# Optimization experiments

Hardware: AMD Instinct MI355X
Metric: run time of the kernel (lower is better)

## Reference

```python
import jax, jax.numpy as jnp
import numpy as np

N, IN, C, H, NC, E, G = 4096, 16, 128, 2, 4, 131072, 64
EPS = 1e-5


def setup_inputs() -> dict:
    key = jax.random.key(0)
    ks = jax.random.split(key, 12)
    def rn(k, shape, scale=0.05):
        return jax.random.normal(k, shape, dtype=jnp.float32) * scale
    return dict(
        x=rn(ks[0], (N, IN), 1.0),
        edge_index=jax.random.randint(ks[1], (2, E), 0, N, dtype=jnp.int32),
        batch=jnp.sort(jax.random.randint(ks[2], (N,), 0, G, dtype=jnp.int32)),
        proj_W=rn(ks[3], (IN, C)), proj_b=jnp.zeros((C,), jnp.float32),
        gcn_W=rn(ks[4], (2, C, C)), gcn_b=jnp.zeros((2, C), jnp.float32),
        attn_qkv_w=rn(ks[5], (2, 3 * C, C)), attn_qkv_b=jnp.zeros((2, 3 * C), jnp.float32),
        attn_out_w=rn(ks[6], (2, C, C)), attn_out_b=jnp.zeros((2, C), jnp.float32),
        bn_gamma=jnp.ones((2, 3, C), jnp.float32), bn_beta=jnp.zeros((2, 3, C), jnp.float32),
        mlp_W1=rn(ks[7], (2, C, 2 * C)), mlp_b1=jnp.zeros((2, 2 * C), jnp.float32),
        mlp_W2=rn(ks[8], (2, 2 * C, C)), mlp_b2=jnp.zeros((2, C), jnp.float32),
        lin_W=rn(ks[9], (C, NC)), lin_b=jnp.zeros((NC,), jnp.float32),
    )


def _bn(h, g, b):
    # PyG BatchNorm (training-mode stats over the node dim, biased var)
    mu = jnp.mean(h, axis=0)
    var = jnp.mean((h - mu) ** 2, axis=0)
    return (h - mu) * jax.lax.rsqrt(var + EPS) * g + b


def _gcn(h_in, W, b, src, dst):
    # GCNConv: x' = D^-1/2 (A+I) D^-1/2 (x W) + b
    h = h_in @ W
    deg = jnp.zeros((N,), h.dtype).at[dst].add(1.0) + 1.0  # +1 self loop
    dinv = jax.lax.rsqrt(deg)
    coef = dinv[src] * dinv[dst]                           # [E]
    out = jax.ops.segment_sum(h[src] * coef[:, None], dst, num_segments=N)
    out = out + h * (dinv * dinv)[:, None]                 # self-loop term
    return out + b


def _mha(x, wqkv, bqkv, wout, bout):
    # batch=None in the source => attention over all N nodes as one sequence
    qkv = x @ wqkv.T + bqkv                                # [N,3C]
    q, k, v = jnp.split(qkv, 3, axis=-1)
    dh = C // H
    q = q.reshape(N, H, dh) * (dh ** -0.5)
    k = k.reshape(N, H, dh)
    v = v.reshape(N, H, dh)
    a = jax.nn.softmax(jnp.einsum('nhd,mhd->hnm', q, k), axis=-1)  # [H,N,N]
    o = jnp.einsum('hnm,mhd->nhd', a, v).reshape(N, C)
    return o @ wout.T + bout


def _forward(x, proj_W, proj_b, gcn_W, gcn_b, attn_qkv_w, attn_qkv_b,
             attn_out_w, attn_out_b, bn_gamma, bn_beta, mlp_W1, mlp_b1,
             mlp_W2, mlp_b2, lin_W, lin_b, edge_index, batch):
    src, dst = edge_index[0], edge_index[1]
    h = x @ proj_W + proj_b
    for l in range(2):  # two structurally-distinct GPS layers
        hl = _bn(_gcn(h, gcn_W[l], gcn_b[l], src, dst) + h, bn_gamma[l, 0], bn_beta[l, 0])
        ha = _bn(_mha(h, attn_qkv_w[l], attn_qkv_b[l], attn_out_w[l], attn_out_b[l]) + h,
                 bn_gamma[l, 1], bn_beta[l, 1])
        o = hl + ha
        m = jax.nn.relu(o @ mlp_W1[l] + mlp_b1[l]) @ mlp_W2[l] + mlp_b2[l]
        h = _bn(o + m, bn_gamma[l, 2], bn_beta[l, 2])
        if l == 0:
            h = jax.nn.relu(h)
    ssum = jax.ops.segment_sum(h, batch, num_segments=G)
    cnt = jax.ops.segment_sum(jnp.ones((N,), h.dtype), batch, num_segments=G)
    pooled = ssum / jnp.maximum(cnt, 1.0)[:, None]
    return pooled @ lin_W + lin_b


def reference(x, edge_index, batch, proj_W, proj_b, gcn_W, gcn_b,
              attn_qkv_w, attn_qkv_b, attn_out_w, attn_out_b,
              bn_gamma, bn_beta, mlp_W1, mlp_b1, mlp_W2, mlp_b2,
              lin_W, lin_b):
    return _forward(x, proj_W, proj_b, gcn_W, gcn_b, attn_qkv_w, attn_qkv_b,
                    attn_out_w, attn_out_b, bn_gamma, bn_beta, mlp_W1, mlp_b1,
                    mlp_W2, mlp_b2, lin_W, lin_b, edge_index, batch)
```

## Files before the change

### kernel.cpp

```cpp
#include <hip/hip_runtime.h>
#include <hip/hip_bf16.h>


constexpr int N_  = 4096;
constexpr int IN_ = 16;
constexpr int C_  = 128;
constexpr int E_  = 131072;
constexpr int G_  = 64;
constexpr float EPSV = 1e-5f;
constexpr int SP_ = 8;

typedef unsigned short u16;
typedef __attribute__((ext_vector_type(8))) short bf16x8;
typedef __attribute__((ext_vector_type(8))) unsigned short u16x8;
typedef __attribute__((ext_vector_type(4))) float f32x4;

__device__ inline u16 f2bf(float f) {
  union { __hip_bfloat16 b; u16 u; } v;
  v.b = __float2bfloat16(f);
  return v.u;
}
__device__ inline float bf2f(u16 s) {
  union { unsigned u; float f; } v; v.u = ((unsigned)s) << 16;
  return v.f;
}

__global__ __launch_bounds__(256) void prol_k(const float* __restrict__ x,
                                              const float* __restrict__ projW,
                                              const float* __restrict__ projB,
                                              float* __restrict__ h,
                                              const float* __restrict__ gcnW,
                                              const float* __restrict__ qkvW,
                                              const float* __restrict__ outW,
                                              const float* __restrict__ w1,
                                              const float* __restrict__ w2,
                                              u16* __restrict__ Wh,
                                              u16* __restrict__ Wl,
                                              const int* __restrict__ ei,
                                              int* __restrict__ cnt) {
  const int bx = blockIdx.x;
  const int tid = threadIdx.x;
  if (bx < 2048) {
    int idx = bx * 256 + tid;
    int n = idx >> 7, c = idx & 127;
    float acc = projB[c];
#pragma unroll
    for (int k = 0; k < IN_; ++k) acc = fmaf(x[n * IN_ + k], projW[k * C_ + c], acc);
    h[idx] = acc;
    return;
  }
  if (bx >= 2336) {
    int e = (bx - 2336) * 256 + tid;
    atomicAdd(&cnt[ei[E_ + e]], 1);
    return;
  }
  int wb = bx - 2048;
  int l = wb / 144, b = wb % 144;
  const float* src; int dstOff, K, M, trans;
  if (b < 16)       { src = gcnW + l * 16384; dstOff = 0;      K = 128; M = 128; trans = 0; }
  else if (b < 64)  { src = qkvW + l * 49152; dstOff = 16384;  K = 128; M = 0;   trans = 1; b -= 16; }
  else if (b < 80)  { src = outW + l * 16384; dstOff = 65536;  K = 128; M = 0;   trans = 1; b -= 64; }
  else if (b < 112) { src = w1 + l * 32768;   dstOff = 81920;  K = 128; M = 256; trans = 0; b -= 80; }
  else              { src = w2 + l * 32768;   dstOff = 114688; K = 256; M = 128; trans = 0; b -= 112; }
  dstOff += l * 147456;
  int d = b * 1024 + tid * 4;
  float v[4];
  if (trans) {
    const float4 f = *(const float4*)&src[d];
    v[0] = f.x; v[1] = f.y; v[2] = f.z; v[3] = f.w;
  } else {
    int ks = (K == 256) ? 8 : 7;
    int n = d >> ks, k = d & (K - 1);
#pragma unroll
    for (int j = 0; j < 4; ++j) v[j] = src[(size_t)(k + j) * M + n];
  }
  ushort4 hv, lv;
  u16* hp = (u16*)&hv; u16* lp = (u16*)&lv;
#pragma unroll
  for (int j = 0; j < 4; ++j) {
    u16 hh = f2bf(v[j]); hp[j] = hh; lp[j] = f2bf(v[j] - bf2f(hh));
  }
  *(ushort4*)&Wh[dstOff + d] = hv;
  *(ushort4*)&Wl[dstOff + d] = lv;
}

__global__ __launch_bounds__(256) void scan_k(const int* __restrict__ cnt,
                                              int* __restrict__ rowptr,
                                              int* __restrict__ cursor,
                                              float* __restrict__ dinv) {
  __shared__ int part[256];
  const int t = threadIdx.x;
  int v[16], s = 0;
#pragma unroll
  for (int i = 0; i < 16; ++i) { v[i] = cnt[t * 16 + i]; s += v[i]; }
  part[t] = s;
  __syncthreads();
  if (t == 0) {
    int run = 0;
    for (int i = 0; i < 256; ++i) { int x = part[i]; part[i] = run; run += x; }
  }
  __syncthreads();
  int off = part[t];
#pragma unroll
  for (int i = 0; i < 16; ++i) {
    int n = t * 16 + i;
    rowptr[n] = off; cursor[n] = off;
    dinv[n] = rsqrtf((float)v[i] + 1.0f);
    off += v[i];
  }
  if (t == 0) rowptr[N_] = E_;
}

__global__ __launch_bounds__(256) void mgemm_dual_k(const float* __restrict__ A,
                                                    const u16* __restrict__ Bh,
                                                    const u16* __restrict__ Bl,
                                                    const float* __restrict__ qkvB,
                                                    float* __restrict__ t0,
                                                    u16* __restrict__ Qg,
                                                    u16* __restrict__ Kg,
                                                    u16* __restrict__ Vtg,
                                                    const int* __restrict__ ei,
                                                    int* __restrict__ cursor,
                                                    int* __restrict__ csr) {
  constexpr int LD = 72, K = 128;
  __shared__ u16 Ah[64 * LD], Al[64 * LD], Bsh[64 * LD], Bsl[64 * LD];
  const int bx = blockIdx.x;
  const int tid = threadIdx.x;
  if (bx >= 512) {
    int e = (bx - 512) * 256 + tid;
    int d = ei[E_ + e];
    int slot = atomicAdd(&cursor[d], 1);
    csr[slot] = ei[e];
    return;
  }
  const int row0 = (bx >> 3) * 64, col0 = (bx & 7) * 64;
  const int wv = tid >> 6, ln = tid & 63, quad = ln >> 4, c = ln & 15;
  f32x4 acc[4];
#pragma unroll
  for (int i = 0; i < 4; ++i) acc[i] = (f32x4){0.f, 0.f, 0.f, 0.f};

  for (int kt = 0; kt < K; kt += 64) {
    __syncthreads();
#pragma unroll
    for (int i = 0; i < 2; ++i) {
      int ch = tid + i * 256, r = ch >> 3, part = ch & 7;
      const float4 f0 = *(const float4*)&A[(size_t)(row0 + r) * K + kt + part * 8];
      const float4 f1 = *(const float4*)&A[(size_t)(row0 + r) * K + kt + part * 8 + 4];
      float fv[8] = {f0.x, f0.y, f0.z, f0.w, f1.x, f1.y, f1.z, f1.w};
      __attribute__((aligned(16))) u16 hb[8], lb[8];
#pragma unroll
      for (int j = 0; j < 8; ++j) {
        u16 hh = f2bf(fv[j]); hb[j] = hh; lb[j] = f2bf(fv[j] - bf2f(hh));
      }
      *(u16x8*)&Ah[r * LD + part * 8] = *(u16x8*)hb;
      *(u16x8*)&Al[r * LD + part * 8] = *(u16x8*)lb;
      size_t bo = (size_t)(col0 + r) * K + kt + part * 8;
      *(u16x8*)&Bsh[r * LD + part * 8] = *(const u16x8*)&Bh[bo];
      *(u16x8*)&Bsl[r * LD + part * 8] = *(const u16x8*)&Bl[bo];
    }
    __syncthreads();
#pragma unroll
    for (int kq = 0; kq < 2; ++kq) {
      bf16x8 ah = *(const bf16x8*)&Ah[(wv * 16 + c) * LD + kq * 32 + quad * 8];
      bf16x8 al = *(const bf16x8*)&Al[(wv * 16 + c) * LD + kq * 32 + quad * 8];
#pragma unroll
      for (int cb = 0; cb < 4; ++cb) {
        bf16x8 bh = *(const bf16x8*)&Bsh[(cb * 16 + c) * LD + kq * 32 + quad * 8];
        bf16x8 bl = *(const bf16x8*)&Bsl[(cb * 16 + c) * LD + kq * 32 + quad * 8];
        acc[cb] = __builtin_amdgcn_mfma_f32_16x16x32_bf16(al, bh, acc[cb], 0, 0, 0);
        acc[cb] = __builtin_amdgcn_mfma_f32_16x16x32_bf16(ah, bl, acc[cb], 0, 0, 0);
        acc[cb] = __builtin_amdgcn_mfma_f32_16x16x32_bf16(ah, bh, acc[cb], 0, 0, 0);
      }
    }
  }

  const int cls = bx & 7;
  if (cls < 2) {
#pragma unroll
    for (int cb = 0; cb < 4; ++cb)
#pragma unroll
      for (int r = 0; r < 4; ++r) {
        int rr = row0 + wv * 16 + quad * 4 + r;
        t0[(size_t)rr * 128 + col0 + cb * 16 + c] = acc[cb][r];
      }
  } else if (cls < 6) {
    const int isQ = cls < 4, hd = cls & 1;
    const float sc = isQ ? 0.125f : 1.0f;
    u16* dst = isQ ? Qg : Kg;
#pragma unroll
    for (int cb = 0; cb < 4; ++cb) {
      int d = cb * 16 + c;
      float qb = qkvB[col0 - 128 + d];
#pragma unroll
      for (int r = 0; r < 4; ++r) {
        int rr = row0 + wv * 16 + quad * 4 + r;
        dst[((size_t)(hd * N_ + rr)) * 64 + d] = f2bf((acc[cb][r] + qb) * sc);
      }
    }
  } else {
    const int hd = cls & 1;
    u16* vtile = Ah;
    __syncthreads();
#pragma unroll
    for (int cb = 0; cb < 4; ++cb) {
      int d = cb * 16 + c;
      float vb = qkvB[col0 - 128 + d];
#pragma unroll
      for (int r = 0; r < 4; ++r)
        vtile[(wv * 16 + quad * 4 + r) * LD + d] = f2bf(acc[cb][r] + vb);
    }
    __syncthreads();
    int d = tid >> 2, j = tid & 3;
    __attribute__((aligned(16))) u16 buf[16];
#pragma unroll
    for (int m = 0; m < 16; ++m) buf[m] = vtile[(j * 16 + m) * LD + d];
    size_t o = ((size_t)(hd * 64 + d)) * N_ + row0 + j * 16;
    *(u16x8*)&Vtg[o]     = *(u16x8*)&buf[0];
    *(u16x8*)&Vtg[o + 8] = *(u16x8*)&buf[8];
  }
}

__global__ __launch_bounds__(256) void mgemm_k(const float* __restrict__ A,
                                               const u16* __restrict__ Bh,
                                               const u16* __restrict__ Bl,
                                               const float* __restrict__ bias,
                                               float* __restrict__ Cout,
                                               int K, int Ncols, int relu,
                                               const float* __restrict__ resid,
                                               float* __restrict__ sums) {
  constexpr int LD = 72;
  __shared__ u16 Ah[64 * LD], Al[64 * LD], Bsh[64 * LD], Bsl[64 * LD];
  const int tid = threadIdx.x;
  const int row0 = blockIdx.y * 64, col0 = blockIdx.x * 64;
  const int wv = tid >> 6, ln = tid & 63, quad = ln >> 4, c = ln & 15;
  f32x4 acc[4];
#pragma unroll
  for (int i = 0; i < 4; ++i) acc[i] = (f32x4){0.f, 0.f, 0.f, 0.f};

  for (int kt = 0; kt < K; kt += 64) {
    __syncthreads();
#pragma unroll
    for (int i = 0; i < 2; ++i) {
      int ch = tid + i * 256, r = ch >> 3, part = ch & 7;
      const float4 f0 = *(const float4*)&A[(size_t)(row0 + r) * K + kt + part * 8];
      const float4 f1 = *(const float4*)&A[(size_t)(row0 + r) * K + kt + part * 8 + 4];
      float fv[8] = {f0.x, f0.y, f0.z, f0.w, f1.x, f1.y, f1.z, f1.w};
      __attribute__((aligned(16))) u16 hb[8], lb[8];
#pragma unroll
      for (int j = 0; j < 8; ++j) {
        u16 hh = f2bf(fv[j]); hb[j] = hh; lb[j] = f2bf(fv[j] - bf2f(hh));
      }
      *(u16x8*)&Ah[r * LD + part * 8] = *(u16x8*)hb;
      *(u16x8*)&Al[r * LD + part * 8] = *(u16x8*)lb;
      size_t bo = (size_t)(col0 + r) * K + kt + part * 8;
      *(u16x8*)&Bsh[r * LD + part * 8] = *(const u16x8*)&Bh[bo];
      *(u16x8*)&Bsl[r * LD + part * 8] = *(const u16x8*)&Bl[bo];
    }
    __syncthreads();
#pragma unroll
    for (int kq = 0; kq < 2; ++kq) {
      bf16x8 ah = *(const bf16x8*)&Ah[(wv * 16 + c) * LD + kq * 32 + quad * 8];
      bf16x8 al = *(const bf16x8*)&Al[(wv * 16 + c) * LD + kq * 32 + quad * 8];
#pragma unroll
      for (int cb = 0; cb < 4; ++cb) {
        bf16x8 bh = *(const bf16x8*)&Bsh[(cb * 16 + c) * LD + kq * 32 + quad * 8];
        bf16x8 bl = *(const bf16x8*)&Bsl[(cb * 16 + c) * LD + kq * 32 + quad * 8];
        acc[cb] = __builtin_amdgcn_mfma_f32_16x16x32_bf16(al, bh, acc[cb], 0, 0, 0);
        acc[cb] = __builtin_amdgcn_mfma_f32_16x16x32_bf16(ah, bl, acc[cb], 0, 0, 0);
        acc[cb] = __builtin_amdgcn_mfma_f32_16x16x32_bf16(ah, bh, acc[cb], 0, 0, 0);
      }
    }
  }
#pragma unroll
  for (int cb = 0; cb < 4; ++cb) {
    float s = 0.0f, s2 = 0.0f;
#pragma unroll
    for (int r = 0; r < 4; ++r) {
      int rr = row0 + wv * 16 + quad * 4 + r;
      int cc = col0 + cb * 16 + c;
      float o = acc[cb][r] + (bias ? bias[cc] : 0.0f);
      if (resid) o += resid[(size_t)rr * Ncols + cc];
      if (relu) o = fmaxf(o, 0.0f);
      Cout[(size_t)rr * Ncols + cc] = o;
      s += o; s2 = fmaf(o, o, s2);
    }
    if (sums) {
      s  += __shfl_xor(s, 16);  s  += __shfl_xor(s, 32);
      s2 += __shfl_xor(s2, 16); s2 += __shfl_xor(s2, 32);
      if (quad == 0) {
        int cc = col0 + cb * 16 + c;
        atomicAdd(&sums[cc], s);
        atomicAdd(&sums[C_ + cc], s2);
      }
    }
  }
}

__global__ __launch_bounds__(256) void mgemm_attn_k(const float* __restrict__ attnP,
                                                    const float* __restrict__ accLp,
                                                    const u16* __restrict__ Bh,
                                                    const u16* __restrict__ Bl,
                                                    const float* __restrict__ bias,
                                                    float* __restrict__ Cout,
                                                    const float* __restrict__ resid,
                                                    float* __restrict__ sums) {
  constexpr int LD = 72, K = 128;
  __shared__ u16 Ah[64 * LD], Al[64 * LD], Bsh[64 * LD], Bsl[64 * LD];
  const int tid = threadIdx.x;
  const int row0 = blockIdx.y * 64, col0 = blockIdx.x * 64;
  const int wv = tid >> 6, ln = tid & 63, quad = ln >> 4, c = ln & 15;
  f32x4 acc[4];
#pragma unroll
  for (int i = 0; i < 4; ++i) acc[i] = (f32x4){0.f, 0.f, 0.f, 0.f};

  for (int kt = 0; kt < K; kt += 64) {
    const int head = kt >> 6;
    __syncthreads();
#pragma unroll
    for (int i = 0; i < 2; ++i) {
      int ch = tid + i * 256, r = ch >> 3, part = ch & 7;
      float lsum = 0.0f;
#pragma unroll
      for (int sp = 0; sp < SP_; ++sp) lsum += accLp[(sp * 2 + head) * N_ + row0 + r];
      float invl = 1.0f / lsum;
      float fv[8] = {0.f, 0.f, 0.f, 0.f, 0.f, 0.f, 0.f, 0.f};
#pragma unroll
      for (int sp = 0; sp < SP_; ++sp) {
        const float* p = &attnP[((size_t)sp * N_ + row0 + r) * C_ + kt + part * 8];
        const float4 f0 = *(const float4*)p;
        const float4 f1 = *(const float4*)(p + 4);
        fv[0] += f0.x; fv[1] += f0.y; fv[2] += f0.z; fv[3] += f0.w;
        fv[4] += f1.x; fv[5] += f1.y; fv[6] += f1.z; fv[7] += f1.w;
      }
      __attribute__((aligned(16))) u16 hb[8], lb[8];
#pragma unroll
      for (int j = 0; j < 8; ++j) {
        float f = fv[j] * invl;
        u16 hh = f2bf(f); hb[j] = hh; lb[j] = f2bf(f - bf2f(hh));
      }
      *(u16x8*)&Ah[r * LD + part * 8] = *(u16x8*)hb;
      *(u16x8*)&Al[r * LD + part * 8] = *(u16x8*)lb;
      size_t bo = (size_t)(col0 + r) * K + kt + part * 8;
      *(u16x8*)&Bsh[r * LD + part * 8] = *(const u16x8*)&Bh[bo];
      *(u16x8*)&Bsl[r * LD + part * 8] = *(const u16x8*)&Bl[bo];
    }
    __syncthreads();
#pragma unroll
    for (int kq = 0; kq < 2; ++kq) {
      bf16x8 ah = *(const bf16x8*)&Ah[(wv * 16 + c) * LD + kq * 32 + quad * 8];
      bf16x8 al = *(const bf16x8*)&Al[(wv * 16 + c) * LD + kq * 32 + quad * 8];
#pragma unroll
      for (int cb = 0; cb < 4; ++cb) {
        bf16x8 bh = *(const bf16x8*)&Bsh[(cb * 16 + c) * LD + kq * 32 + quad * 8];
        bf16x8 bl = *(const bf16x8*)&Bsl[(cb * 16 + c) * LD + kq * 32 + quad * 8];
        acc[cb] = __builtin_amdgcn_mfma_f32_16x16x32_bf16(al, bh, acc[cb], 0, 0, 0);
        acc[cb] = __builtin_amdgcn_mfma_f32_16x16x32_bf16(ah, bl, acc[cb], 0, 0, 0);
        acc[cb] = __builtin_amdgcn_mfma_f32_16x16x32_bf16(ah, bh, acc[cb], 0, 0, 0);
      }
    }
  }
#pragma unroll
  for (int cb = 0; cb < 4; ++cb) {
    float s = 0.0f, s2 = 0.0f;
#pragma unroll
    for (int r = 0; r < 4; ++r) {
      int rr = row0 + wv * 16 + quad * 4 + r;
      int cc = col0 + cb * 16 + c;
      float o = acc[cb][r] + bias[cc] + resid[(size_t)rr * 128 + cc];
      Cout[(size_t)rr * 128 + cc] = o;
      s += o; s2 = fmaf(o, o, s2);
    }
    s  += __shfl_xor(s, 16);  s  += __shfl_xor(s, 32);
    s2 += __shfl_xor(s2, 16); s2 += __shfl_xor(s2, 32);
    if (quad == 0) {
      int cc = col0 + cb * 16 + c;
      atomicAdd(&sums[cc], s);
      atomicAdd(&sums[C_ + cc], s2);
    }
  }
}

__global__ __launch_bounds__(256) void branch_k(const u16* __restrict__ Qg,
                                                const u16* __restrict__ Kg,
                                                const u16* __restrict__ Vtg,
                                                float* __restrict__ attnP,
                                                float* __restrict__ accLp,
                                                const int* __restrict__ rowptr,
                                                const int* __restrict__ csr,
                                                const float* __restrict__ hw,
                                                const float* __restrict__ dinv,
                                                const float* __restrict__ gbias,
                                                const float* __restrict__ hres,
                                                float* __restrict__ t1,
                                                float* __restrict__ sums0) {
  constexpr int LD = 72;
  __shared__ __attribute__((aligned(16))) u16 smem[3 * 64 * LD];
  const int tid = threadIdx.x;
  const int bx = blockIdx.x;

  if (bx & 1) {
    const int b = bx >> 1;
    const int wq = tid >> 6, lane = tid & 63;
    const int n = b * 4 + wq;
    float* ls  = (float*)smem;
    float* ls2 = ls + 512;
    const float din = dinv[n];
    float a0 = fmaf(hw[(size_t)n * C_ + lane], din * din,
                    gbias[lane] + hres[(size_t)n * C_ + lane]);
    float a1 = fmaf(hw[(size_t)n * C_ + lane + 64], din * din,
                    gbias[lane + 64] + hres[(size_t)n * C_ + lane + 64]);
    const int e1 = rowptr[n + 1];
    for (int e = rowptr[n]; e < e1; ++e) {
      int si = csr[e];
      float w = dinv[si] * din;
      a0 = fmaf(hw[(size_t)si * C_ + lane], w, a0);
      a1 = fmaf(hw[(size_t)si * C_ + lane + 64], w, a1);
    }
    t1[(size_t)n * C_ + lane]      = a0;
    t1[(size_t)n * C_ + lane + 64] = a1;
    ls[wq * 128 + lane]       = a0;  ls[wq * 128 + lane + 64]  = a1;
    ls2[wq * 128 + lane]      = a0 * a0;
    ls2[wq * 128 + lane + 64] = a1 * a1;
    __syncthreads();
    if (tid < 128) {
      float s  = ls[tid]  + ls[tid + 128]  + ls[tid + 256]  + ls[tid + 384];
      float s2 = ls2[tid] + ls2[tid + 128] + ls2[tid + 256] + ls2[tid + 384];
      atomicAdd(&sums0[tid], s);
      atomicAdd(&sums0[C_ + tid], s2);
    }
    return;
  }

  u16* Ks  = smem;
  u16* Vts = smem + 64 * LD;
  u16* Ps  = smem + 2 * 64 * LD;
  const int fb = bx >> 1;
  const int head = fb >> 9, sp = (fb >> 6) & 7, q0 = (fb & 63) * 64;
  const int wv = tid >> 6, ln = tid & 63, quad = ln >> 4, c = ln & 15;
  const int KPS = N_ / SP_;

  bf16x8 qf[2];
#pragma unroll
  for (int kq = 0; kq < 2; ++kq)
    qf[kq] = *(const bf16x8*)&Qg[((size_t)(head * N_ + q0 + wv * 16 + c)) * 64 + kq * 32 + quad * 8];

  f32x4 O[4];
#pragma unroll
  for (int i = 0; i < 4; ++i) O[i] = (f32x4){0.f, 0.f, 0.f, 0.f};
  float l4[4] = {0.f, 0.f, 0.f, 0.f};
  u16* Pw = &Ps[wv * 16 * LD];

  for (int it = 0; it < KPS / 64; ++it) {
    const int k0 = sp * KPS + it * 64;
    __syncthreads();
#pragma unroll
    for (int i = 0; i < 2; ++i) {
      int ch = tid + i * 256, row = ch >> 3, part = ch & 7;
      *(u16x8*)&Ks[row * LD + part * 8] =
          *(const u16x8*)&Kg[((size_t)(head * N_ + k0 + row)) * 64 + part * 8];
      *(u16x8*)&Vts[row * LD + part * 8] =
          *(const u16x8*)&Vtg[((size_t)(head * 64 + row)) * N_ + k0 + part * 8];
    }
    __syncthreads();

#pragma unroll
    for (int kb = 0; kb < 4; ++kb) {
      f32x4 s = (f32x4){0.f, 0.f, 0.f, 0.f};
#pragma unroll
      for (int kq = 0; kq < 2; ++kq) {
        bf16x8 b = *(const bf16x8*)&Ks[(kb * 16 + c) * LD + kq * 32 + quad * 8];
        s = __builtin_amdgcn_mfma_f32_16x16x32_bf16(qf[kq], b, s, 0, 0, 0);
      }
#pragma unroll
      for (int r = 0; r < 4; ++r) {
        u16 ph = f2bf(__expf(s[r] - 8.0f));
        l4[r] += bf2f(ph);
        Pw[(quad * 4 + r) * LD + kb * 16 + c] = ph;
      }
    }
#pragma unroll
    for (int db = 0; db < 4; ++db) {
#pragma unroll
      for (int kq = 0; kq < 2; ++kq) {
        bf16x8 a = *(const bf16x8*)&Pw[c * LD + kq * 32 + quad * 8];
        bf16x8 b = *(const bf16x8*)&Vts[(db * 16 + c) * LD + kq * 32 + quad * 8];
        O[db] = __builtin_amdgcn_mfma_f32_16x16x32_bf16(a, b, O[db], 0, 0, 0);
      }
    }
  }

#pragma unroll
  for (int r = 0; r < 4; ++r) {
#pragma unroll
    for (int off = 1; off < 16; off <<= 1) l4[r] += __shfl_xor(l4[r], off);
  }

#pragma unroll
  for (int db = 0; db < 4; ++db)
#pragma unroll
    for (int r = 0; r < 4; ++r) {
      int q = q0 + wv * 16 + quad * 4 + r;
      attnP[((size_t)sp * N_ + q) * C_ + head * 64 + db * 16 + c] = O[db][r];
    }
  if (c == 0) {
#pragma unroll
    for (int r = 0; r < 4; ++r)
      accLp[(sp * 2 + head) * N_ + q0 + wv * 16 + quad * 4 + r] = l4[r];
  }
}

__global__ __launch_bounds__(256) void bn_finapply2_k(const float* __restrict__ t0,
                                                      const float* __restrict__ t1,
                                                      const float* __restrict__ sums1,
                                                      const float* __restrict__ sums0,
                                                      const float* __restrict__ g1,
                                                      const float* __restrict__ b1v,
                                                      const float* __restrict__ g0,
                                                      const float* __restrict__ b0v,
                                                      float* __restrict__ ob) {
  __shared__ float scl1[128], shf1[128], scl0[128], shf0[128];
  const int t = threadIdx.x;
  if (t < 128) {
    float mu = sums1[t] * (1.0f / N_);
    float var = sums1[C_ + t] * (1.0f / N_) - mu * mu;
    float sc = rsqrtf(var + EPSV) * g1[t];
    scl1[t] = sc; shf1[t] = fmaf(-mu, sc, b1v[t]);
    mu = sums0[t] * (1.0f / N_);
    var = sums0[C_ + t] * (1.0f / N_) - mu * mu;
    sc = rsqrtf(var + EPSV) * g0[t];
    scl0[t] = sc; shf0[t] = fmaf(-mu, sc, b0v[t]);
  }
  __syncthreads();
  int idx = blockIdx.x * 256 + t;
  int c = idx & 127;
  ob[idx] = fmaf(t0[idx], scl1[c], shf1[c]) + fmaf(t1[idx], scl0[c], shf0[c]);
}

__global__ __launch_bounds__(256) void bn_finapply_k(const float* __restrict__ A,
                                                     const float* __restrict__ sums,
                                                     const float* __restrict__ g,
                                                     const float* __restrict__ b,
                                                     float* __restrict__ outp, int relu,
                                                     const int* __restrict__ batch,
                                                     float* __restrict__ pooled) {
  __shared__ float s_scl[128], s_shf[128];
  const int t = threadIdx.x;
  if (t < 128) {
    float mu = sums[t] * (1.0f / N_);
    float var = sums[C_ + t] * (1.0f / N_) - mu * mu;
    float sc = rsqrtf(var + EPSV) * g[t];
    s_scl[t] = sc;
    s_shf[t] = fmaf(-mu, sc, b[t]);
  }
  __syncthreads();
  int idx = blockIdx.x * 256 + t;
  int c = idx & 127;
  float v = fmaf(A[idx], s_scl[c], s_shf[c]);
  if (relu) v = fmaxf(v, 0.0f);
  outp[idx] = v;
  if (pooled) {
    int n = idx >> 7;
    atomicAdd(&pooled[(size_t)batch[n] * C_ + c], v);
  }
}

__global__ __launch_bounds__(256) void final_k(const float* __restrict__ pooled,
                                               const int* __restrict__ batch,
                                               const float* __restrict__ W,
                                               const float* __restrict__ b,
                                               float* __restrict__ out) {
  int t = threadIdx.x;
  int g = t >> 2, j = t & 3;
  int lo = 0, hi = N_;
  while (lo < hi) { int m = (lo + hi) >> 1; if (batch[m] < g) lo = m + 1; else hi = m; }
  int st = lo; lo = 0; hi = N_;
  while (lo < hi) { int m = (lo + hi) >> 1; if (batch[m] < g + 1) lo = m + 1; else hi = m; }
  float inv = 1.0f / fmaxf((float)(lo - st), 1.0f);
  float acc = b[j];
  for (int c = 0; c < C_; ++c) acc = fmaf(pooled[(size_t)g * C_ + c] * inv, W[c * 4 + j], acc);
  out[t] = acc;
}

extern "C" void kernel_launch(void* const* d_in, const int* in_sizes, int n_in,
                              void* d_out, int out_size, void* d_ws, size_t ws_size,
                              hipStream_t stream) {
  const float* x     = (const float*)d_in[0];
  const int*   ei    = (const int*)d_in[1];
  const int*   batch = (const int*)d_in[2];
  const float* projW = (const float*)d_in[3];
  const float* projB = (const float*)d_in[4];
  const float* gcnW  = (const float*)d_in[5];
  const float* gcnB  = (const float*)d_in[6];
  const float* qkvW  = (const float*)d_in[7];
  const float* qkvB  = (const float*)d_in[8];
  const float* outW  = (const float*)d_in[9];
  const float* outB  = (const float*)d_in[10];
  const float* bnG   = (const float*)d_in[11];
  const float* bnB   = (const float*)d_in[12];
  const float* w1    = (const float*)d_in[13];
  const float* b1    = (const float*)d_in[14];
  const float* w2    = (const float*)d_in[15];
  const float* b2    = (const float*)d_in[16];
  const float* linW  = (const float*)d_in[17];
  const float* linB  = (const float*)d_in[18];
  float* out = (float*)d_out;

  const size_t NC = (size_t)N_ * C_;
  const size_t HB = (size_t)2 * N_ * 64;
  float* ws   = (float*)d_ws;
  float* h    = ws;
  float* t0   = ws + 1 * NC;
  float* t1   = ws + 2 * NC;
  float* ob   = ws + 3 * NC;
  u16* Qg  = (u16*)(ws + 4 * NC);
  u16* Kg  = Qg + HB;
  u16* Vtg = Kg + HB;
  float* attnP = ws + 6 * NC;
  float* m1b   = attnP;
  float* accLp = ws + (6 + SP_) * NC;
  float* sums  = accLp + 2 * SP_ * N_;
  float* pooled = sums + 6 * 256;
  int*   icnt = (int*)(pooled + (size_t)G_ * C_);
  float* dinv = (float*)(icnt + N_);
  int*   rowptr = (int*)(dinv + N_);
  int*   cursor = rowptr + N_ + 1;
  int*   csr    = cursor + N_;
  u16*   Wh = (u16*)(csr + E_);
  u16*   Wl = Wh + 2 * 147456;

  const dim3 b256(256);

  hipMemsetAsync(sums, 0, (6 * 256 + (size_t)G_ * C_ + N_) * sizeof(float), stream);

  prol_k<<<2848, b256, 0, stream>>>(x, projW, projB, h, gcnW, qkvW, outW,
                                    w1, w2, Wh, Wl, ei, icnt);
  scan_k<<<1, b256, 0, stream>>>(icnt, rowptr, cursor, dinv);

  for (int l = 0; l < 2; ++l) {
    const size_t WL = (size_t)l * 147456;
    float* sums0 = sums + (l * 3 + 0) * 256;
    float* sums1 = sums + (l * 3 + 1) * 256;
    float* sums2 = sums + (l * 3 + 2) * 256;

    mgemm_dual_k<<<(l == 0) ? 1024 : 512, b256, 0, stream>>>(
        h, Wh + WL, Wl + WL, qkvB + l * 384, t0, Qg, Kg, Vtg, ei, cursor, csr);
    branch_k<<<2048, b256, 0, stream>>>(Qg, Kg, Vtg, attnP, accLp,
                                        rowptr, csr, t0, dinv, gcnB + l * C_,
                                        h, t1, sums0);
    mgemm_attn_k<<<dim3(2, 64), b256, 0, stream>>>(attnP, accLp,
                                                   Wh + WL + 65536, Wl + WL + 65536,
                                                   outB + l * C_, t0, h, sums1);
    bn_finapply2_k<<<(int)(NC / 256), b256, 0, stream>>>(
        t0, t1, sums1, sums0,
        bnG + (l * 3 + 1) * C_, bnB + (l * 3 + 1) * C_,
        bnG + (l * 3 + 0) * C_, bnB + (l * 3 + 0) * C_, ob);
    mgemm_k<<<dim3(4, 64), b256, 0, stream>>>(ob, Wh + WL + 81920, Wl + WL + 81920,
                                              b1 + l * 256, m1b, 128, 256, 1,
                                              nullptr, nullptr);
    mgemm_k<<<dim3(2, 64), b256, 0, stream>>>(m1b, Wh + WL + 114688, Wl + WL + 114688,
                                              b2 + l * C_, t0, 256, 128, 0,
                                              ob, sums2);
    bn_finapply_k<<<(int)(NC / 256), b256, 0, stream>>>(
        t0, sums2, bnG + (l * 3 + 2) * C_, bnB + (l * 3 + 2) * C_, h,
        (l == 0) ? 1 : 0, batch, (l == 1) ? pooled : nullptr);
  }

  final_k<<<1, 256, 0, stream>>>(pooled, batch, linW, linB, out);
}
```

Baseline: 318.4 us.

## Keep attention P in registers via transposed MFMA and bpermute, vectorize output stores

The attention path computes S^T by swapping the MFMA operands, so each lane holds probabilities for a single query. These are packed as bf16 pairs and redistributed with ds_bpermute to form the B operand of the PV MFMA, replacing the LDS round trip for P and shrinking shared memory. The per-row exp sum becomes one scalar per lane reduced with two shuffles. Output tiles are transposed through LDS so attnP is written with float4 stores. The GCN gather loop is also unrolled by four to get more loads in flight.

```diff
diff --git a/kernel.cpp b/kernel.cpp
--- a/kernel.cpp
+++ b/kernel.cpp
@@ -11,6 +11,7 @@
 constexpr int SP_ = 8;
 
 typedef unsigned short u16;
+typedef unsigned int u32;
 typedef __attribute__((ext_vector_type(8))) short bf16x8;
 typedef __attribute__((ext_vector_type(8))) unsigned short u16x8;
 typedef __attribute__((ext_vector_type(4))) float f32x4;
@@ -394,7 +395,7 @@
                                                 float* __restrict__ t1,
                                                 float* __restrict__ sums0) {
   constexpr int LD = 72;
-  __shared__ __attribute__((aligned(16))) u16 smem[3 * 64 * LD];
+  __shared__ __attribute__((aligned(16))) u16 smem[2 * 64 * LD];
   const int tid = threadIdx.x;
   const int bx = blockIdx.x;
 
@@ -410,7 +411,21 @@
     float a1 = fmaf(hw[(size_t)n * C_ + lane + 64], din * din,
                     gbias[lane + 64] + hres[(size_t)n * C_ + lane + 64]);
     const int e1 = rowptr[n + 1];
-    for (int e = rowptr[n]; e < e1; ++e) {
+    int e = rowptr[n];
+    for (; e + 4 <= e1; e += 4) {
+      int s0 = csr[e], s1 = csr[e + 1], s2i = csr[e + 2], s3 = csr[e + 3];
+      float w0 = dinv[s0] * din, w1 = dinv[s1] * din;
+      float w2 = dinv[s2i] * din, w3 = dinv[s3] * din;
+      float x00 = hw[(size_t)s0 * C_ + lane],  x01 = hw[(size_t)s0 * C_ + lane + 64];
+      float x10 = hw[(size_t)s1 * C_ + lane],  x11 = hw[(size_t)s1 * C_ + lane + 64];
+      float x20 = hw[(size_t)s2i * C_ + lane], x21 = hw[(size_t)s2i * C_ + lane + 64];
+      float x30 = hw[(size_t)s3 * C_ + lane],  x31 = hw[(size_t)s3 * C_ + lane + 64];
+      a0 = fmaf(x00, w0, a0); a1 = fmaf(x01, w0, a1);
+      a0 = fmaf(x10, w1, a0); a1 = fmaf(x11, w1, a1);
+      a0 = fmaf(x20, w2, a0); a1 = fmaf(x21, w2, a1);
+      a0 = fmaf(x30, w3, a0); a1 = fmaf(x31, w3, a1);
+    }
+    for (; e < e1; ++e) {
       int si = csr[e];
       float w = dinv[si] * din;
       a0 = fmaf(hw[(size_t)si * C_ + lane], w, a0);
@@ -433,7 +448,6 @@
 
   u16* Ks  = smem;
   u16* Vts = smem + 64 * LD;
-  u16* Ps  = smem + 2 * 64 * LD;
   const int fb = bx >> 1;
   const int head = fb >> 9, sp = (fb >> 6) & 7, q0 = (fb & 63) * 64;
   const int wv = tid >> 6, ln = tid & 63, quad = ln >> 4, c = ln & 15;
@@ -447,8 +461,11 @@
   f32x4 O[4];
 #pragma unroll
   for (int i = 0; i < 4; ++i) O[i] = (f32x4){0.f, 0.f, 0.f, 0.f};
-  float l4[4] = {0.f, 0.f, 0.f, 0.f};
-  u16* Pw = &Ps[wv * 16 * LD];
+  float lsum = 0.0f;
+
+  const int ad0 = (c | (((quad << 1) & 3) << 4)) << 2;
+  const int ad1 = (c | ((((quad << 1) | 1) & 3) << 4)) << 2;
+  const bool hiq = quad >= 2;
 
   for (int it = 0; it < KPS / 64; ++it) {
     const int k0 = sp * KPS + it * 64;
@@ -463,49 +480,68 @@
     }
     __syncthreads();
 
+    u32 pk[4][2];
 #pragma unroll
     for (int kb = 0; kb < 4; ++kb) {
-      f32x4 s = (f32x4){0.f, 0.f, 0.f, 0.f};
+      f32x4 st = (f32x4){0.f, 0.f, 0.f, 0.f};
 #pragma unroll
       for (int kq = 0; kq < 2; ++kq) {
-        bf16x8 b = *(const bf16x8*)&Ks[(kb * 16 + c) * LD + kq * 32 + quad * 8];
-        s = __builtin_amdgcn_mfma_f32_16x16x32_bf16(qf[kq], b, s, 0, 0, 0);
-      }
-#pragma unroll
-      for (int r = 0; r < 4; ++r) {
-        u16 ph = f2bf(__expf(s[r] - 8.0f));
-        l4[r] += bf2f(ph);
-        Pw[(quad * 4 + r) * LD + kb * 16 + c] = ph;
-      }
-    }
-#pragma unroll
-    for (int db = 0; db < 4; ++db) {
-#pragma unroll
-      for (int kq = 0; kq < 2; ++kq) {
-        bf16x8 a = *(const bf16x8*)&Pw[c * LD + kq * 32 + quad * 8];
-        bf16x8 b = *(const bf16x8*)&Vts[(db * 16 + c) * LD + kq * 32 + quad * 8];
-        O[db] = __builtin_amdgcn_mfma_f32_16x16x32_bf16(a, b, O[db], 0, 0, 0);
-      }
-    }
-  }
-
-#pragma unroll
-  for (int r = 0; r < 4; ++r) {
-#pragma unroll
-    for (int off = 1; off < 16; off <<= 1) l4[r] += __shfl_xor(l4[r], off);
-  }
-
+        bf16x8 a = *(const bf16x8*)&Ks[(kb * 16 + c) * LD + kq * 32 + quad * 8];
+        st = __builtin_amdgcn_mfma_f32_16x16x32_bf16(a, qf[kq], st, 0, 0, 0);
+      }
+      u16 p0 = f2bf(__expf(st[0] - 8.0f));
+      u16 p1 = f2bf(__expf(st[1] - 8.0f));
+      u16 p2 = f2bf(__expf(st[2] - 8.0f));
+      u16 p3 = f2bf(__expf(st[3] - 8.0f));
+      lsum += bf2f(p0) + bf2f(p1) + bf2f(p2) + bf2f(p3);
+      pk[kb][0] = (u32)p0 | ((u32)p1 << 16);
+      pk[kb][1] = (u32)p2 | ((u32)p3 << 16);
+    }
+
+#pragma unroll
+    for (int kq = 0; kq < 2; ++kq) {
+      union { u32 w[4]; bf16x8 v; } pt;
+      {
+        u32 aA = __builtin_amdgcn_ds_bpermute(ad0, (int)pk[2 * kq][0]);
+        u32 aB = __builtin_amdgcn_ds_bpermute(ad0, (int)pk[2 * kq + 1][0]);
+        pt.w[0] = hiq ? aB : aA;
+        u32 bA = __builtin_amdgcn_ds_bpermute(ad0, (int)pk[2 * kq][1]);
+        u32 bB = __builtin_amdgcn_ds_bpermute(ad0, (int)pk[2 * kq + 1][1]);
+        pt.w[1] = hiq ? bB : bA;
+        u32 cA = __builtin_amdgcn_ds_bpermute(ad1, (int)pk[2 * kq][0]);
+        u32 cB = __builtin_amdgcn_ds_bpermute(ad1, (int)pk[2 * kq + 1][0]);
+        pt.w[2] = hiq ? cB : cA;
+        u32 dA = __builtin_amdgcn_ds_bpermute(ad1, (int)pk[2 * kq][1]);
+        u32 dB = __builtin_amdgcn_ds_bpermute(ad1, (int)pk[2 * kq + 1][1]);
+        pt.w[3] = hiq ? dB : dA;
+      }
+#pragma unroll
+      for (int db = 0; db < 4; ++db) {
+        bf16x8 vb = *(const bf16x8*)&Vts[(db * 16 + c) * LD + kq * 32 + quad * 8];
+        O[db] = __builtin_amdgcn_mfma_f32_16x16x32_bf16(vb, pt.v, O[db], 0, 0, 0);
+      }
+    }
+  }
+
+  lsum += __shfl_xor(lsum, 16);
+  lsum += __shfl_xor(lsum, 32);
+  if (ln < 16)
+    accLp[(sp * 2 + head) * N_ + q0 + wv * 16 + c] = lsum;
+
+  __syncthreads();
+  float* OT = (float*)smem;
 #pragma unroll
   for (int db = 0; db < 4; ++db)
 #pragma unroll
-    for (int r = 0; r < 4; ++r) {
-      int q = q0 + wv * 16 + quad * 4 + r;
-      attnP[((size_t)sp * N_ + q) * C_ + head * 64 + db * 16 + c] = O[db][r];
-    }
-  if (c == 0) {
-#pragma unroll
     for (int r = 0; r < 4; ++r)
-      accLp[(sp * 2 + head) * N_ + q0 + wv * 16 + quad * 4 + r] = l4[r];
+      OT[(wv * 16 + c) * LD + db * 16 + quad * 4 + r] = O[db][r];
+  __syncthreads();
+  {
+    const int q_loc = tid >> 2, dblk = tid & 3;
+    const float4* srcv = (const float4*)&OT[q_loc * LD + dblk * 16];
+    float4* dstv = (float4*)&attnP[((size_t)sp * N_ + q0 + q_loc) * C_ + head * 64 + dblk * 16];
+#pragma unroll
+    for (int j = 0; j < 4; ++j) dstv[j] = srcv[j];
   }
 }
 
```

After: 333.3 us. 1.05x slower.
